# Optimization experiments

Hardware: AMD Instinct MI355X
Metric: run time of the kernel (lower is better)

Reference implementation:

```python
import jax, jax.numpy as jnp
import numpy as np

C = 1.0          # Poincare ball curvature
TEMP = 0.1       # softmax temperature
EPS = 1e-15
TANH_CLIP = 1.0 - 1e-5


def setup_inputs() -> dict:
    key = jax.random.key(0)
    ks = jax.random.split(key, 9)
    B, Din, H, D, P = 2048, 1024, 4096, 128, 1000
    inp = {
        "x": jax.random.normal(ks[0], (B, Din), dtype=jnp.float32),
        "W1": jax.random.normal(ks[1], (Din, H), dtype=jnp.float32) / np.sqrt(Din),
        "b1": jnp.zeros((H,), dtype=jnp.float32),
        "W2": jax.random.normal(ks[2], (H, H), dtype=jnp.float32) / np.sqrt(H),
        "b2": jnp.zeros((H,), dtype=jnp.float32),
        "W3": jax.random.normal(ks[3], (H, D), dtype=jnp.float32) / np.sqrt(H),
        "b3": jnp.zeros((D,), dtype=jnp.float32),
        # prototypes: points inside the unit ball (norm ~ 0.2)
        "prototypes": jax.random.normal(ks[4], (P, D), dtype=jnp.float32) * 0.02,
    }
    return inp


def _expmap0(u):
    sqc = np.sqrt(C)
    n = jnp.maximum(jnp.linalg.norm(u, axis=-1, keepdims=True), EPS)
    return jnp.tanh(sqc * n) * u / (sqc * n)


def _logmap0(y):
    sqc = np.sqrt(C)
    n = jnp.maximum(jnp.linalg.norm(y, axis=-1, keepdims=True), EPS)
    arg = jnp.clip(sqc * n, 0.0, TANH_CLIP)
    return jnp.arctanh(arg) * y / (sqc * n)


def _pairwise_dist(proto, xh):
    # dist(x=proto[P,D], y=xh[B,D]) = (2/sqrt(c)) * artanh(sqrt(c)*||(-x) (+) y||)
    # Mobius add norm computed from Gram products only (no [B,P,D] intermediate).
    # a = -proto, b = xh
    a2 = jnp.sum(proto * proto, axis=-1)          # [P]  ||a||^2
    b2 = jnp.sum(xh * xh, axis=-1)                # [B]  ||b||^2
    ab = -jnp.einsum('bd,pd->bp', xh, proto)      # [B,P] <a,b>
    a2_ = a2[None, :]
    b2_ = b2[:, None]
    alpha = 1.0 + 2.0 * C * ab + C * b2_
    beta = 1.0 - C * a2_
    gamma = 1.0 + 2.0 * C * ab + (C * C) * a2_ * b2_
    m2 = (alpha * alpha * a2_ + 2.0 * alpha * beta * ab + beta * beta * b2_) / (gamma * gamma)
    mnorm = jnp.sqrt(jnp.maximum(m2, 0.0))
    sqc = np.sqrt(C)
    arg = jnp.clip(sqc * mnorm, 0.0, TANH_CLIP)
    return (2.0 / sqc) * jnp.arctanh(arg)         # [B,P]


def reference(x, W1, b1, W2, b2, W3, b3, prototypes):
    h = jax.nn.gelu(x @ W1 + b1, approximate=False)
    h = jax.nn.gelu(h @ W2 + b2, approximate=False)
    u = h @ W3 + b3                               # [B,D]
    x_hyp = _expmap0(u)
    dists = _pairwise_dist(prototypes, x_hyp)     # [B,P]
    logits = -dists / TEMP
    pred = jnp.argmax(logits, axis=1)             # [B]
    pred_protos = jax.lax.stop_gradient(prototypes[pred])  # detach, as in torch
    feedback = _logmap0(pred_protos)              # [B,D]
    return logits, feedback
```

## Files before the change

### kernel.cpp

```cpp
#include <hip/hip_runtime.h>
#include <math.h>

#define B_SZ 2048
#define DIN  1024
#define H_SZ 4096
#define D_SZ 128
#define P_SZ 1000

typedef __attribute__((ext_vector_type(8))) short bf16x8;
typedef __attribute__((ext_vector_type(4))) float f32x4;

__device__ __forceinline__ float gelu_exact(float v) {
    return 0.5f * v * (1.0f + erff(v * 0.70710678118654752f));
}

__device__ __forceinline__ short f2bf(float f) {
    unsigned u = __float_as_uint(f);
    u = (u + 0x7fffu + ((u >> 16) & 1u)) >> 16;
    return (short)u;
}

__device__ __forceinline__ void gload_lds16(const void* g, void* l) {
    __builtin_amdgcn_global_load_lds(
        (__attribute__((address_space(1))) void*)(uintptr_t)g,
        (__attribute__((address_space(3))) void*)(uintptr_t)l,
        16, 0, 0);
}

__global__ __launch_bounds__(256) void cvt_bf16(
    const float* __restrict__ in, short* __restrict__ out, int n)
{
    const int i = (blockIdx.x * 256 + threadIdx.x) * 4;
    if (i + 3 < n) {
        const float4 v = *reinterpret_cast<const float4*>(&in[i]);
        short4 o;
        o.x = f2bf(v.x); o.y = f2bf(v.y); o.z = f2bf(v.z); o.w = f2bf(v.w);
        *reinterpret_cast<short4*>(&out[i]) = o;
    }
}

__global__ __launch_bounds__(256) void transpose_bf16(
    const float* __restrict__ W, short* __restrict__ WT, int K, int N)
{
    __shared__ float t[64][65];
    const int tid = threadIdx.x;
    const int tx = tid & 63, ty = tid >> 6;
    const int n0 = blockIdx.x * 64, k0 = blockIdx.y * 64;
    #pragma unroll
    for (int r = 0; r < 64; r += 4)
        t[r + ty][tx] = W[(size_t)(k0 + r + ty) * N + n0 + tx];
    __syncthreads();
    #pragma unroll
    for (int r = 0; r < 64; r += 4)
        WT[(size_t)(n0 + r + ty) * K + k0 + tx] = f2bf(t[tx][r + ty]);
}

__global__ __launch_bounds__(512) void gemm_big(
    const short* __restrict__ A, const short* __restrict__ BT,
    const float* __restrict__ bias, short* __restrict__ Cout,
    int M, int N, int K)
{
    extern __shared__ __align__(16) char smem[];

    const int tid  = threadIdx.x;
    const int lane = tid & 63;
    const int wid  = tid >> 6;
    const int row0 = blockIdx.y * 256;
    const int col0 = blockIdx.x * 128;
    const int wm = (wid >> 1) * 64;
    const int wn = (wid & 1) * 64;
    const int lr = lane & 15, kq = lane >> 4;

    const int NT = K >> 6;

    f32x4 acc[4][4];
    #pragma unroll
    for (int i = 0; i < 4; ++i)
        #pragma unroll
        for (int j = 0; j < 4; ++j) acc[i][j] = (f32x4){0.f, 0.f, 0.f, 0.f};

    const int srow = lane >> 3;
    const int kch  = (lane & 7) ^ srow;
    const short* Ag = A  + (size_t)(row0 + wid * 32 + srow) * K + kch * 8;
    const short* Bg = BT + (size_t)(col0 + wid * 16 + srow) * K + kch * 8;

    auto stage = [&](int t) {
        const int buf = t % 3;
        char* sA = smem + buf * 49152;
        char* sB = sA + 32768;
        const int k0 = t << 6;
        #pragma unroll
        for (int ii = 0; ii < 4; ++ii)
            gload_lds16(Ag + (size_t)ii * 8 * K + k0, sA + (wid * 4 + ii) * 1024);
        #pragma unroll
        for (int ii = 0; ii < 2; ++ii)
            gload_lds16(Bg + (size_t)ii * 8 * K + k0, sB + (wid * 2 + ii) * 1024);
    };

    stage(0);
    stage(1);
    asm volatile("s_waitcnt vmcnt(6)" ::: "memory");
    __builtin_amdgcn_s_barrier();
    asm volatile("" ::: "memory");

    for (int t = 0; t < NT; ++t) {
        const bool more = (t + 2) < NT;
        if (more) stage(t + 2);

        const char* sA = smem + (t % 3) * 49152;
        const char* sB = sA + 32768;

        #pragma unroll
        for (int ks = 0; ks < 2; ++ks) {
            bf16x8 af[4], bfv[4];
            #pragma unroll
            for (int i = 0; i < 4; ++i) {
                const int row = wm + i * 16 + lr;
                af[i] = *reinterpret_cast<const bf16x8*>(
                    sA + row * 128 + (((ks * 4 + kq) ^ (lr & 7)) * 16));
            }
            #pragma unroll
            for (int j = 0; j < 4; ++j) {
                const int row = wn + j * 16 + lr;
                bfv[j] = *reinterpret_cast<const bf16x8*>(
                    sB + row * 128 + (((ks * 4 + kq) ^ (lr & 7)) * 16));
            }
            __builtin_amdgcn_s_setprio(1);
            #pragma unroll
            for (int i = 0; i < 4; ++i)
                #pragma unroll
                for (int j = 0; j < 4; ++j)
                    acc[i][j] = __builtin_amdgcn_mfma_f32_16x16x32_bf16(
                        af[i], bfv[j], acc[i][j], 0, 0, 0);
            __builtin_amdgcn_s_setprio(0);
        }

        asm volatile("" ::: "memory");
        if (more) asm volatile("s_waitcnt vmcnt(6) lgkmcnt(0)" ::: "memory");
        else      asm volatile("s_waitcnt vmcnt(0) lgkmcnt(0)" ::: "memory");
        __builtin_amdgcn_s_barrier();
        asm volatile("" ::: "memory");
    }

    #pragma unroll
    for (int j = 0; j < 4; ++j) {
        const int col = col0 + wn + j * 16 + lr;
        const float bv = bias[col];
        #pragma unroll
        for (int i = 0; i < 4; ++i) {
            #pragma unroll
            for (int q = 0; q < 4; ++q) {
                const int row = row0 + wm + i * 16 + kq * 4 + q;
                float v = gelu_exact(acc[i][j][q] + bv);
                Cout[(size_t)row * N + col] = f2bf(v);
            }
        }
    }
}

__global__ __launch_bounds__(256) void gemm_small_splitk(
    const short* __restrict__ A, const short* __restrict__ BT,
    float* __restrict__ Cout, int M, int N, int K)
{
    __shared__ __align__(16) short sA[4 * 128 * 8];
    __shared__ __align__(16) short sB[4 * 128 * 8];

    const int tid  = threadIdx.x;
    const int lane = tid & 63;
    const int wid  = tid >> 6;
    const int row0 = blockIdx.y * 128;
    const int col0 = blockIdx.x * 128;
    const int wm = (wid >> 1) * 64;
    const int wn = (wid & 1) * 64;

    const int kpb    = K / gridDim.z;
    const int kstart = blockIdx.z * kpb;

    f32x4 acc[4][4];
    #pragma unroll
    for (int i = 0; i < 4; ++i)
        #pragma unroll
        for (int j = 0; j < 4; ++j) acc[i][j] = (f32x4){0.f, 0.f, 0.f, 0.f};

    const short* Ab = A  + (size_t)(row0 + lane) * K;
    const short* Bb = BT + (size_t)(col0 + lane) * K;
    short* ldsA = &sA[wid * (128 * 8)];
    short* ldsB = &sB[wid * (128 * 8)];

    const int kq = lane >> 4;
    const int lr = lane & 15;

    for (int k0 = kstart; k0 < kstart + kpb; k0 += 32) {
        gload_lds16(Ab + k0 + wid * 8,                  ldsA);
        gload_lds16(Ab + (size_t)64 * K + k0 + wid * 8, ldsA + 64 * 8);
        gload_lds16(Bb + k0 + wid * 8,                  ldsB);
        gload_lds16(Bb + (size_t)64 * K + k0 + wid * 8, ldsB + 64 * 8);
        __syncthreads();

        bf16x8 af[4], bfr[4];
        #pragma unroll
        for (int i = 0; i < 4; ++i)
            af[i] = *reinterpret_cast<const bf16x8*>(&sA[kq * (128 * 8) + (wm + i * 16 + lr) * 8]);
        #pragma unroll
        for (int j = 0; j < 4; ++j)
            bfr[j] = *reinterpret_cast<const bf16x8*>(&sB[kq * (128 * 8) + (wn + j * 16 + lr) * 8]);

        #pragma unroll
        for (int i = 0; i < 4; ++i)
            #pragma unroll
            for (int j = 0; j < 4; ++j)
                acc[i][j] = __builtin_amdgcn_mfma_f32_16x16x32_bf16(af[i], bfr[j], acc[i][j], 0, 0, 0);
        __syncthreads();
    }

    #pragma unroll
    for (int j = 0; j < 4; ++j) {
        const int col = col0 + wn + j * 16 + lr;
        if (col < N) {
            #pragma unroll
            for (int i = 0; i < 4; ++i)
                #pragma unroll
                for (int q = 0; q < 4; ++q) {
                    const int row = row0 + wm + i * 16 + kq * 4 + q;
                    atomicAdd(&Cout[(size_t)row * N + col], acc[i][j][q]);
                }
        }
    }
}

__global__ __launch_bounds__(128) void expmap_kernel(
    float* __restrict__ uxh, const float* __restrict__ b3, float* __restrict__ rowb2)
{
    const int b = blockIdx.x;
    const int d = threadIdx.x;
    float u = uxh[(size_t)b * D_SZ + d] + b3[d];

    float s = u * u;
    #pragma unroll
    for (int off = 32; off; off >>= 1) s += __shfl_down(s, off);
    __shared__ float part[2];
    if ((d & 63) == 0) part[d >> 6] = s;
    __syncthreads();
    const float n2 = part[0] + part[1];

    const float n = fmaxf(sqrtf(n2), 1e-15f);
    const float t = tanhf(n);
    uxh[(size_t)b * D_SZ + d] = u * (t / n);
    if (d == 0) rowb2[b] = t * t;
}

__global__ __launch_bounds__(128) void a2_kernel(
    const float* __restrict__ proto, float* __restrict__ a2g)
{
    const int p = blockIdx.x;
    const int d = threadIdx.x;
    const float y = proto[(size_t)p * D_SZ + d];
    float s = y * y;
    #pragma unroll
    for (int off = 32; off; off >>= 1) s += __shfl_down(s, off);
    __shared__ float part[2];
    if ((d & 63) == 0) part[d >> 6] = s;
    __syncthreads();
    if (d == 0) a2g[p] = part[0] + part[1];
}

__global__ __launch_bounds__(256) void dist_kernel(
    const float* __restrict__ xh, const float* __restrict__ proto,
    const float* __restrict__ rowb2, const float* __restrict__ a2g,
    float* __restrict__ logits)
{
    __shared__ float xs[128][68];
    __shared__ float ps[128][68];
    __shared__ float sb2[64], sa2[64];

    const int tid = threadIdx.x;
    const int pt = blockIdx.x * 64;
    const int bt = blockIdx.y * 64;

    #pragma unroll
    for (int r = 0; r < 8; ++r) {
        const int idx = r * 256 + tid;
        const int row = idx >> 5;
        const int dq  = (idx & 31) * 4;
        const float4 v = *reinterpret_cast<const float4*>(&xh[(size_t)(bt + row) * D_SZ + dq]);
        xs[dq + 0][row] = v.x; xs[dq + 1][row] = v.y; xs[dq + 2][row] = v.z; xs[dq + 3][row] = v.w;
        const int prow = pt + row;
        float4 w = {0.f, 0.f, 0.f, 0.f};
        if (prow < P_SZ) w = *reinterpret_cast<const float4*>(&proto[(size_t)prow * D_SZ + dq]);
        ps[dq + 0][row] = w.x; ps[dq + 1][row] = w.y; ps[dq + 2][row] = w.z; ps[dq + 3][row] = w.w;
    }
    if (tid < 64) {
        sb2[tid] = rowb2[bt + tid];
        sa2[tid] = (pt + tid < P_SZ) ? a2g[pt + tid] : 0.f;
    }
    __syncthreads();

    const int tx = tid & 15, ty = tid >> 4;
    float dot[4][4] = {};
    for (int d = 0; d < 128; ++d) {
        const float4 a4 = *reinterpret_cast<const float4*>(&xs[d][ty * 4]);
        const float4 b4 = *reinterpret_cast<const float4*>(&ps[d][tx * 4]);
        const float aa[4] = {a4.x, a4.y, a4.z, a4.w};
        const float bb[4] = {b4.x, b4.y, b4.z, b4.w};
        #pragma unroll
        for (int i = 0; i < 4; ++i)
            #pragma unroll
            for (int j = 0; j < 4; ++j)
                dot[i][j] = fmaf(aa[i], bb[j], dot[i][j]);
    }

    #pragma unroll
    for (int i = 0; i < 4; ++i) {
        const int b = bt + ty * 4 + i;
        const float b2 = sb2[ty * 4 + i];
        #pragma unroll
        for (int j = 0; j < 4; ++j) {
            const int p = pt + tx * 4 + j;
            if (p < P_SZ) {
                const float a2 = sa2[tx * 4 + j];
                const float ab = -dot[i][j];
                const float alpha = 1.f + 2.f * ab + b2;
                const float beta  = 1.f - a2;
                const float gamma = 1.f + 2.f * ab + a2 * b2;
                const float num = alpha * alpha * a2 + 2.f * alpha * beta * ab + beta * beta * b2;
                const float m2 = num / (gamma * gamma);
                const float mn = sqrtf(fmaxf(m2, 0.f));
                const float arg = fminf(mn, 0.99999f);
                const float dist = logf((1.f + arg) / (1.f - arg));
                logits[(size_t)b * P_SZ + p] = -10.f * dist;
            }
        }
    }
}

__global__ __launch_bounds__(256) void head_kernel(
    const float* __restrict__ logits, const float* __restrict__ proto,
    float* __restrict__ fb)
{
    const int b = blockIdx.x;
    const int tid = threadIdx.x;

    float best = -INFINITY; int bi = 0;
    for (int p = tid; p < P_SZ; p += 256) {
        const float v = logits[(size_t)b * P_SZ + p];
        if (v > best) { best = v; bi = p; }
    }
    __shared__ float bv[256];
    __shared__ int   bidx[256];
    bv[tid] = best; bidx[tid] = bi;
    __syncthreads();
    for (int s = 128; s; s >>= 1) {
        if (tid < s) {
            const float ov = bv[tid + s]; const int oi = bidx[tid + s];
            if (ov > bv[tid] || (ov == bv[tid] && oi < bidx[tid])) { bv[tid] = ov; bidx[tid] = oi; }
        }
        __syncthreads();
    }
    const int pred = bidx[0];
    __syncthreads();

    float y = 0.f;
    if (tid < 128) y = proto[(size_t)pred * D_SZ + tid];
    bv[tid] = y * y;
    __syncthreads();
    for (int s = 128; s; s >>= 1) {
        if (tid < s) bv[tid] += bv[tid + s];
        __syncthreads();
    }
    const float n2 = bv[0];
    if (tid < 128) {
        const float n = fmaxf(sqrtf(n2), 1e-15f);
        const float arg = fminf(n, 0.99999f);
        const float at = 0.5f * logf((1.f + arg) / (1.f - arg));
        fb[(size_t)b * D_SZ + tid] = at * (y / n);
    }
}

extern "C" void kernel_launch(void* const* d_in, const int* in_sizes, int n_in,
                              void* d_out, int out_size, void* d_ws, size_t ws_size,
                              hipStream_t stream)
{
    const float* x     = (const float*)d_in[0];
    const float* W1    = (const float*)d_in[1];
    const float* b1    = (const float*)d_in[2];
    const float* W2    = (const float*)d_in[3];
    const float* b2v   = (const float*)d_in[4];
    const float* W3    = (const float*)d_in[5];
    const float* b3    = (const float*)d_in[6];
    const float* proto = (const float*)d_in[7];

    float* logits = (float*)d_out;
    float* fb     = logits + (size_t)B_SZ * P_SZ;

    short* xb    = (short*)d_ws;
    short* w1t   = xb   + (size_t)B_SZ * DIN;
    short* w2t   = w1t  + (size_t)H_SZ * DIN;
    short* w3t   = w2t  + (size_t)H_SZ * H_SZ;
    short* h1    = w3t  + (size_t)D_SZ * H_SZ;
    short* h2    = h1   + (size_t)B_SZ * H_SZ;
    float* u     = (float*)(h2 + (size_t)B_SZ * H_SZ);
    float* rowb2 = u + (size_t)B_SZ * D_SZ;
    float* a2g   = rowb2 + B_SZ;

    static_cast<void>(hipFuncSetAttribute(
        reinterpret_cast<const void*>(&gemm_big),
        hipFuncAttributeMaxDynamicSharedMemorySize, 3 * 49152));

    cvt_bf16<<<(B_SZ * DIN) / 1024, 256, 0, stream>>>(x, xb, B_SZ * DIN);
    transpose_bf16<<<dim3(H_SZ / 64, DIN / 64), 256, 0, stream>>>(W1, w1t, DIN, H_SZ);
    transpose_bf16<<<dim3(H_SZ / 64, H_SZ / 64), 256, 0, stream>>>(W2, w2t, H_SZ, H_SZ);
    transpose_bf16<<<dim3(D_SZ / 64, H_SZ / 64), 256, 0, stream>>>(W3, w3t, H_SZ, D_SZ);

    gemm_big<<<dim3(H_SZ / 128, B_SZ / 256), 512, 3 * 49152, stream>>>(
        xb, w1t, b1, h1, B_SZ, H_SZ, DIN);
    gemm_big<<<dim3(H_SZ / 128, B_SZ / 256), 512, 3 * 49152, stream>>>(
        h1, w2t, b2v, h2, B_SZ, H_SZ, H_SZ);
    hipMemsetAsync(u, 0, (size_t)B_SZ * D_SZ * sizeof(float), stream);
    gemm_small_splitk<<<dim3(1, B_SZ / 128, 8), 256, 0, stream>>>(
        h2, w3t, u, B_SZ, D_SZ, H_SZ);

    expmap_kernel<<<B_SZ, 128, 0, stream>>>(u, b3, rowb2);
    a2_kernel<<<P_SZ, 128, 0, stream>>>(proto, a2g);
    dist_kernel<<<dim3((P_SZ + 63) / 64, B_SZ / 64), 256, 0, stream>>>(u, proto, rowb2, a2g, logits);
    head_kernel<<<B_SZ, 256, 0, stream>>>(logits, proto, fb);
}
```

Measured before the change: 301.3 us.

## Swizzle GEMM block order across XCDs and restructure main loop into ping-pong phases

The big GEMM kernel remaps block indices so consecutive blocks land on the same XCD-chunk for better L2 locality. It also splits each K-tile into two phases, each reading LDS fragments, then issuing its MFMAs between barriers with setprio and sched_barrier. The goal is to interleave LDS reads, global prefetch issue and MFMA across waves. It adds extra barriers per iteration, which could cost more synchronization than it saves.

```diff
diff --git a/kernel.cpp b/kernel.cpp
--- a/kernel.cpp
+++ b/kernel.cpp
@@ -65,8 +65,13 @@
     const int tid  = threadIdx.x;
     const int lane = tid & 63;
     const int wid  = tid >> 6;
-    const int row0 = blockIdx.y * 256;
-    const int col0 = blockIdx.x * 128;
+
+    const int nwg = gridDim.x * gridDim.y;
+    const int bid = blockIdx.y * gridDim.x + blockIdx.x;
+    const int swz = (bid & 7) * (nwg >> 3) + (bid >> 3);
+    const int row0 = (swz / gridDim.x) * 256;
+    const int col0 = (swz % gridDim.x) * 128;
+
     const int wm = (wid >> 1) * 64;
     const int wn = (wid & 1) * 64;
     const int lr = lane & 15, kq = lane >> 4;
@@ -97,6 +102,18 @@
             gload_lds16(Bg + (size_t)ii * 8 * K + k0, sB + (wid * 2 + ii) * 1024);
     };
 
+    auto read_frags = [&](const char* sA, const char* sB, int ks,
+                          bf16x8* af, bf16x8* bfv) {
+        #pragma unroll
+        for (int i = 0; i < 4; ++i)
+            af[i] = *reinterpret_cast<const bf16x8*>(
+                sA + (wm + i * 16 + lr) * 128 + (((ks * 4 + kq) ^ (lr & 7)) * 16));
+        #pragma unroll
+        for (int j = 0; j < 4; ++j)
+            bfv[j] = *reinterpret_cast<const bf16x8*>(
+                sB + (wn + j * 16 + lr) * 128 + (((ks * 4 + kq) ^ (lr & 7)) * 16));
+    };
+
     stage(0);
     stage(1);
     asm volatile("s_waitcnt vmcnt(6)" ::: "memory");
@@ -105,41 +122,43 @@
 
     for (int t = 0; t < NT; ++t) {
         const bool more = (t + 2) < NT;
-        if (more) stage(t + 2);
-
         const char* sA = smem + (t % 3) * 49152;
         const char* sB = sA + 32768;
-
-        #pragma unroll
-        for (int ks = 0; ks < 2; ++ks) {
-            bf16x8 af[4], bfv[4];
-            #pragma unroll
-            for (int i = 0; i < 4; ++i) {
-                const int row = wm + i * 16 + lr;
-                af[i] = *reinterpret_cast<const bf16x8*>(
-                    sA + row * 128 + (((ks * 4 + kq) ^ (lr & 7)) * 16));
-            }
-            #pragma unroll
-            for (int j = 0; j < 4; ++j) {
-                const int row = wn + j * 16 + lr;
-                bfv[j] = *reinterpret_cast<const bf16x8*>(
-                    sB + row * 128 + (((ks * 4 + kq) ^ (lr & 7)) * 16));
-            }
-            __builtin_amdgcn_s_setprio(1);
-            #pragma unroll
-            for (int i = 0; i < 4; ++i)
-                #pragma unroll
-                for (int j = 0; j < 4; ++j)
-                    acc[i][j] = __builtin_amdgcn_mfma_f32_16x16x32_bf16(
-                        af[i], bfv[j], acc[i][j], 0, 0, 0);
-            __builtin_amdgcn_s_setprio(0);
-        }
-
+        bf16x8 af[4], bfv[4];
+
+        read_frags(sA, sB, 0, af, bfv);
+        if (more) stage(t + 2);
         asm volatile("" ::: "memory");
-        if (more) asm volatile("s_waitcnt vmcnt(6) lgkmcnt(0)" ::: "memory");
-        else      asm volatile("s_waitcnt vmcnt(0) lgkmcnt(0)" ::: "memory");
         __builtin_amdgcn_s_barrier();
+        asm volatile("s_waitcnt lgkmcnt(0)" ::: "memory");
+        __builtin_amdgcn_sched_barrier(0);
+        __builtin_amdgcn_s_setprio(1);
+        #pragma unroll
+        for (int i = 0; i < 4; ++i)
+            #pragma unroll
+            for (int j = 0; j < 4; ++j)
+                acc[i][j] = __builtin_amdgcn_mfma_f32_16x16x32_bf16(
+                    af[i], bfv[j], acc[i][j], 0, 0, 0);
+        __builtin_amdgcn_s_setprio(0);
         asm volatile("" ::: "memory");
+        __builtin_amdgcn_s_barrier();
+
+        read_frags(sA, sB, 1, af, bfv);
+        if (more) asm volatile("s_waitcnt vmcnt(6)" ::: "memory");
+        else      asm volatile("s_waitcnt vmcnt(0)" ::: "memory");
+        __builtin_amdgcn_s_barrier();
+        asm volatile("s_waitcnt lgkmcnt(0)" ::: "memory");
+        __builtin_amdgcn_sched_barrier(0);
+        __builtin_amdgcn_s_setprio(1);
+        #pragma unroll
+        for (int i = 0; i < 4; ++i)
+            #pragma unroll
+            for (int j = 0; j < 4; ++j)
+                acc[i][j] = __builtin_amdgcn_mfma_f32_16x16x32_bf16(
+                    af[i], bfv[j], acc[i][j], 0, 0, 0);
+        __builtin_amdgcn_s_setprio(0);
+        asm volatile("" ::: "memory");
+        __builtin_amdgcn_s_barrier();
     }
 
     #pragma unroll
```

New measurement: 308.5 us. +2.4%, slower.
